# Kernel optimization log

Hardware: AMD Instinct MI355X
Metric: run time of the kernel (lower is better)

The kernel has to match this reference:

```python
import jax, jax.numpy as jnp
import numpy as np

B, N, C, H, W = 4, 5, 64, 96, 288
DOWNSAMPLE_RATE = 4
DISCRETE_RATIO = 0.4
DECAY_WEIGHTS = jax.nn.softmax(jnp.array([1.0, 0.5], dtype=jnp.float32))  # frame=1, decay=0.5


def _warp_one(img, theta):
    # img: (C,H,W), theta: (2,3). Matches F.affine_grid + F.grid_sample
    # (bilinear, zeros padding, align_corners=True).
    c, h, w = img.shape
    xs = jnp.linspace(-1.0, 1.0, w, dtype=img.dtype)
    ys = jnp.linspace(-1.0, 1.0, h, dtype=img.dtype)
    gy, gx = jnp.meshgrid(ys, xs, indexing='ij')
    base = jnp.stack([gx.ravel(), gy.ravel(), jnp.ones(h * w, img.dtype)], 0)  # (3, HW)
    g = theta @ base  # (2, HW) normalized coords
    px = (g[0] + 1.0) * 0.5 * (w - 1)
    py = (g[1] + 1.0) * 0.5 * (h - 1)
    x0 = jnp.floor(px); y0 = jnp.floor(py)
    wx = px - x0; wy = py - y0
    def tap(yy, xx):
        yi = jnp.clip(yy, 0, h - 1).astype(jnp.int32)
        xi = jnp.clip(xx, 0, w - 1).astype(jnp.int32)
        valid = ((yy >= 0) & (yy <= h - 1) & (xx >= 0) & (xx <= w - 1)).astype(img.dtype)
        return img[:, yi, xi] * valid  # (C, HW)
    out = (tap(y0, x0) * (1 - wx) * (1 - wy)
           + tap(y0, x0 + 1) * wx * (1 - wy)
           + tap(y0 + 1, x0) * (1 - wx) * wy
           + tap(y0 + 1, x0 + 1) * wx * wy)
    return out.reshape(c, h, w)


def _frame_score(hist, mlp_w, mlp_b):
    # hist: (B,N,C,H,W) -> per-pixel ego-vs-neighbor attention score (B,N,1,H,W).
    b, n, c, h, w = hist.shape
    node = hist.reshape(b, n, c, h * w).transpose(0, 3, 1, 2)  # (B, P, N, C)
    ego = node[:, :, 0]          # (B, P, C)
    neigh = node[:, :, 1:]       # (B, P, N-1, C)
    # Query rows are all the repeated ego vector -> one row suffices (identical math).
    s = jnp.einsum('bpc,bpkc->bpk', ego, neigh) / jnp.sqrt(jnp.asarray(c, hist.dtype))
    attn = jax.nn.softmax(s, axis=-1)
    ctx = jnp.einsum('bpk,bpkc->bpc', attn, neigh)
    sc = jax.nn.sigmoid(ctx @ mlp_w.T + mlp_b)                   # (B, P, 1)
    sc = jnp.broadcast_to(sc[:, :, None, :], (b, h * w, n - 1, 1))
    ego_sc = jnp.ones((b, h * w, 1, 1), hist.dtype)
    overall = jnp.concatenate([ego_sc, sc], axis=2)              # (B, P, N, 1)
    return overall.transpose(0, 2, 3, 1).reshape(b, n, 1, h, w)


def _forward(x0, x1, pairwise_t_matrix, mlp_w, mlp_b):
    x0g = x0.reshape(B, N, C, H, W)
    x1g = x1.reshape(B, N, C, H, W)

    # --- TemporalSampling: weighted per-frame scores, threshold, 3x3 max-pool ---
    conf = DECAY_WEIGHTS[0] * _frame_score(x0g, mlp_w, mlp_b) \
         + DECAY_WEIGHTS[1] * _frame_score(x1g, mlp_w, mlp_b)      # (B,N,1,H,W)
    mask = jnp.where(conf > 0.5, jnp.float32(1.0), jnp.float32(0.0))
    mask = jax.lax.reduce_window(mask, -jnp.inf, jax.lax.max,
                                 (1, 1, 1, 3, 3), (1, 1, 1, 1, 1), 'SAME')
    x = x0g * mask  # broadcast over C

    # --- normalize pairwise transform to 2x3 affine matrices ---
    t = pairwise_t_matrix[:, :, :, jnp.array([0, 1])][:, :, :, :, jnp.array([0, 1, 3])]  # (B,L,L,2,3)
    t = t.at[..., 0, 1].mul(H / W)
    t = t.at[..., 1, 0].mul(W / H)
    t = t.at[..., 0, 2].set(t[..., 0, 2] / (DOWNSAMPLE_RATE * DISCRETE_RATIO * W) * 2)
    t = t.at[..., 1, 2].set(t[..., 1, 2] / (DOWNSAMPLE_RATE * DISCRETE_RATIO * H) * 2)
    theta = t[:, 0]  # (B,N,2,3): warp each cav into ego frame

    # --- per-agent warp ---
    warped = jax.vmap(jax.vmap(_warp_one))(x, theta)  # (B,N,C,H,W)

    # --- AttenFusion: per-pixel NxN attention, keep ego row ---
    nf = warped.reshape(B, N, C, H * W).transpose(0, 3, 1, 2)  # (B, P, N, C)
    s = jnp.einsum('bpc,bpkc->bpk', nf[:, :, 0], nf) / jnp.sqrt(jnp.asarray(C, nf.dtype))
    attn = jax.nn.softmax(s, axis=-1)
    ctx = jnp.einsum('bpk,bpkc->bpc', attn, nf)                 # (B, P, C)
    x_fuse = ctx.transpose(0, 2, 1).reshape(B, C, H, W)
    return x_fuse


def setup_inputs() -> dict:
    key = jax.random.key(0)
    k0, k1, k2, k3 = jax.random.split(key, 4)
    x0 = jax.random.normal(k0, (B * N, C, H, W), dtype=jnp.float32)
    x1 = jax.random.normal(k1, (B * N, C, H, W), dtype=jnp.float32)
    eye = jnp.broadcast_to(jnp.eye(4, dtype=jnp.float32), (B, N, N, 4, 4))
    pairwise_t_matrix = eye + 0.01 * jax.random.normal(k2, (B, N, N, 4, 4), dtype=jnp.float32)
    mlp_w = 0.1 * jax.random.normal(k3, (1, C), dtype=jnp.float32)
    mlp_b = jnp.zeros((1,), dtype=jnp.float32)
    record_len = jnp.full((B,), N, dtype=jnp.int32)
    return {"x0": x0, "x1": x1, "pairwise_t_matrix": pairwise_t_matrix,
            "mlp_w": mlp_w, "mlp_b": mlp_b, "record_len": record_len}


def reference(x0, x1, pairwise_t_matrix, mlp_w, mlp_b, record_len):
    # record_len is uniform (=N) and only determines the static regrouping.
    return _forward(x0, x1, pairwise_t_matrix, mlp_w, mlp_b)
```

## Files before the change

kernel.cpp:

```cpp
#include <hip/hip_runtime.h>
#include <cmath>

#define BB 4
#define NN 5
#define CC 64
#define HH 96
#define WW 288
#define PP (HH*WW)
#define QP (PP/4)
#define BP (BB*PP)
#define BQ (BP/4)
#define TPITCH 65


static __device__ __forceinline__ float sigmoidf_(float x) {
    return 1.0f / (1.0f + expf(-x));
}
static __device__ __forceinline__ float4 f4zero() {
    return make_float4(0.f, 0.f, 0.f, 0.f);
}
static __device__ __forceinline__ void fma4s(float4& a, float s, const float4& v) {
    a.x += s * v.x; a.y += s * v.y; a.z += s * v.z; a.w += s * v.w;
}
static __device__ __forceinline__ void fma44(float4& a, const float4& s, const float4& v) {
    a.x += s.x * v.x; a.y += s.y * v.y; a.z += s.z * v.z; a.w += s.w * v.w;
}
static __device__ __forceinline__ float dot4(const float4& a, const float4& b) {
    return a.x*b.x + a.y*b.y + a.z*b.z + a.w*b.w;
}
static __device__ __forceinline__ float score4(const float* dd, const float* mm, float bias) {
    float s0 = dd[0]*0.125f, s1 = dd[1]*0.125f, s2 = dd[2]*0.125f, s3 = dd[3]*0.125f;
    float mx = fmaxf(fmaxf(s0, s1), fmaxf(s2, s3));
    float e0 = expf(s0-mx), e1 = expf(s1-mx), e2 = expf(s2-mx), e3 = expf(s3-mx);
    float inv = 1.0f / (e0+e1+e2+e3);
    float z = (e0*mm[0] + e1*mm[1] + e2*mm[2] + e3*mm[3]) * inv + bias;
    return sigmoidf_(z);
}

static __device__ __forceinline__ void theta_load(
    const float* __restrict__ pmat, int b, int n,
    float& t00, float& t01, float& t02, float& t10, float& t11, float& t12)
{
    const float* m = pmat + ((size_t)(b * NN + 0) * NN + n) * 16;
    t00 = m[0];
    t01 = m[1] * ((float)HH / (float)WW);
    t02 = m[3] * (float)(2.0 / (4.0 * 0.4 * (double)WW));
    t10 = m[4] * ((float)WW / (float)HH);
    t11 = m[5];
    t12 = m[7] * (float)(2.0 / (4.0 * 0.4 * (double)HH));
}

__global__ __launch_bounds__(256) void x1_part_kernel(
    const float4* __restrict__ x1, const float* __restrict__ mlp_w,
    float4* __restrict__ dpart1)
{
    int q   = blockIdx.x * 256 + threadIdx.x;
    int seg = blockIdx.y;
    int b  = q / QP;
    int qp = q - b * QP;
    const float4* base = x1 + (size_t)b * (NN*CC*QP) + qp;

    float4 d[4] = {f4zero(), f4zero(), f4zero(), f4zero()};
    float4 m[4] = {f4zero(), f4zero(), f4zero(), f4zero()};
    #pragma unroll 4
    for (int ci = 0; ci < 16; ci++) {
        int c = seg * 16 + ci;
        float4 e  = base[(size_t)c * QP];
        float  wc = mlp_w[c];
        #pragma unroll
        for (int k = 1; k < NN; k++) {
            float4 v = base[((size_t)k * CC + c) * QP];
            fma44(d[k-1], e, v);
            fma4s(m[k-1], wc, v);
        }
    }
    #pragma unroll
    for (int j = 0; j < 4; j++) {
        dpart1[((size_t)seg * 8 + j)     * BQ + q] = d[j];
        dpart1[((size_t)seg * 8 + 4 + j) * BQ + q] = m[j];
    }
}

__global__ __launch_bounds__(256) void transpose_mask_kernel(
    const float4* __restrict__ x0f4, const float* __restrict__ mlp_w,
    float4* __restrict__ x0t, float* __restrict__ dpx0)
{
    __shared__ float A[64 * TPITCH];
    __shared__ float Bsh[64 * TPITCH];
    __shared__ float redD[256];
    __shared__ float redM[256];
    __shared__ float wlds[64];

    int t   = threadIdx.x;
    int b   = blockIdx.y;
    int pt0 = blockIdx.x * 64;
    int c   = t >> 2, pq = t & 3;
    int pix = t >> 2, cg = t & 3;

    if (t < 64) wlds[t] = mlp_w[t];

    {
        const float4* src = x0f4 + ((size_t)(b*NN + 0) * CC + c) * QP
                                 + blockIdx.x * 16 + pq * 4;
        float4 r[4];
        #pragma unroll
        for (int j = 0; j < 4; j++) r[j] = src[j];
        #pragma unroll
        for (int j = 0; j < 4; j++) {
            int col = pq * 16 + j * 4;
            A[c*TPITCH + col+0] = r[j].x;
            A[c*TPITCH + col+1] = r[j].y;
            A[c*TPITCH + col+2] = r[j].z;
            A[c*TPITCH + col+3] = r[j].w;
        }
    }
    __syncthreads();
    float a[16];
    {
        #pragma unroll
        for (int j = 0; j < 16; j++) a[j] = A[(cg*16 + j)*TPITCH + pix];
        float4* dst = x0t + ((size_t)(b*NN + 0) * PP + pt0 + pix) * 16 + cg * 4;
        #pragma unroll
        for (int jj = 0; jj < 4; jj++)
            dst[jj] = make_float4(a[jj*4+0], a[jj*4+1], a[jj*4+2], a[jj*4+3]);
    }

    for (int k = 1; k < NN; k++) {
        const float4* src = x0f4 + ((size_t)(b*NN + k) * CC + c) * QP
                                 + blockIdx.x * 16 + pq * 4;
        float4 r[4];
        #pragma unroll
        for (int j = 0; j < 4; j++) r[j] = src[j];
        __syncthreads();
        #pragma unroll
        for (int j = 0; j < 4; j++) {
            int col = pq * 16 + j * 4;
            Bsh[c*TPITCH + col+0] = r[j].x;
            Bsh[c*TPITCH + col+1] = r[j].y;
            Bsh[c*TPITCH + col+2] = r[j].z;
            Bsh[c*TPITCH + col+3] = r[j].w;
        }
        __syncthreads();
        float bv[16];
        #pragma unroll
        for (int j = 0; j < 16; j++) bv[j] = Bsh[(cg*16 + j)*TPITCH + pix];
        float4* dst = x0t + ((size_t)(b*NN + k) * PP + pt0 + pix) * 16 + cg * 4;
        #pragma unroll
        for (int jj = 0; jj < 4; jj++)
            dst[jj] = make_float4(bv[jj*4+0], bv[jj*4+1], bv[jj*4+2], bv[jj*4+3]);

        float sd = 0.f, sm = 0.f;
        #pragma unroll
        for (int j = 0; j < 16; j++) {
            sd += a[j] * bv[j];
            sm += wlds[cg*16 + j] * bv[j];
        }
        redD[t] = sd;
        redM[t] = sm;
        __syncthreads();
        if (t < 64) {
            float dd = redD[t*4] + redD[t*4+1] + redD[t*4+2] + redD[t*4+3];
            float mm = redM[t*4] + redM[t*4+1] + redM[t*4+2] + redM[t*4+3];
            int gp = b * PP + pt0 + t;
            dpx0[(size_t)(k-1)   * BP + gp] = dd;
            dpx0[(size_t)(4+k-1) * BP + gp] = mm;
        }
    }
}

__global__ __launch_bounds__(256) void comb_kernel(
    const float4* __restrict__ dpart1, const float4* __restrict__ dpx0,
    const float* __restrict__ mlp_b, float4* __restrict__ premask)
{
    int q = blockIdx.x * 256 + threadIdx.x;
    float bias = mlp_b[0];

    float4 d1[8];
    #pragma unroll
    for (int j = 0; j < 8; j++) {
        float4 s = f4zero();
        #pragma unroll
        for (int seg = 0; seg < 4; seg++) {
            float4 v = dpart1[((size_t)seg * 8 + j) * BQ + q];
            s.x += v.x; s.y += v.y; s.z += v.z; s.w += v.w;
        }
        d1[j] = s;
    }
    float4 d0[8];
    #pragma unroll
    for (int j = 0; j < 8; j++) d0[j] = dpx0[(size_t)j * BQ + q];

    const float W0 = 0.6224593312018546f, W1 = 0.3775406687981454f;
    float4 res;
    #pragma unroll
    for (int kcomp = 0; kcomp < 4; kcomp++) {
        float dd0[4], mm0[4], dd1[4], mm1[4];
        #pragma unroll
        for (int j = 0; j < 4; j++) {
            dd0[j] = ((const float*)&d0[j])[kcomp];
            mm0[j] = ((const float*)&d0[4+j])[kcomp];
            dd1[j] = ((const float*)&d1[j])[kcomp];
            mm1[j] = ((const float*)&d1[4+j])[kcomp];
        }
        float sc0 = score4(dd0, mm0, bias);
        float sc1 = score4(dd1, mm1, bias);
        float conf = W0 * sc0 + W1 * sc1;
        ((float*)&res)[kcomp] = (conf > 0.5f) ? 1.f : 0.f;
    }
    premask[q] = res;
}

__global__ __launch_bounds__(256) void pool_kernel(
    const float* __restrict__ pre, float4* __restrict__ pooled)
{
    int q  = blockIdx.x * 256 + threadIdx.x;
    int b  = q / QP;
    int qp = q - b * QP;
    int p0 = qp * 4;
    int h  = p0 / WW;
    int w0 = p0 - h * WW;
    const float* pb = pre + (size_t)b * PP;
    float m[4] = {0.f, 0.f, 0.f, 0.f};
    #pragma unroll
    for (int dy = -1; dy <= 1; dy++) {
        int y = h + dy;
        if (y < 0 || y >= HH) continue;
        const float* row = pb + y * WW;
        float c_[6];
        float4 mid = *(const float4*)(row + w0);
        c_[0] = (w0 > 0) ? row[w0 - 1] : 0.f;
        c_[1] = mid.x; c_[2] = mid.y; c_[3] = mid.z; c_[4] = mid.w;
        c_[5] = (w0 + 4 < WW) ? row[w0 + 4] : 0.f;
        #pragma unroll
        for (int j = 0; j < 4; j++)
            m[j] = fmaxf(m[j], fmaxf(c_[j], fmaxf(c_[j+1], c_[j+2])));
    }
    pooled[q] = make_float4(m[0], m[1], m[2], m[3]);
}

__global__ __launch_bounds__(256) void fuse_kernel(
    const float4* __restrict__ x0t, const float* __restrict__ pmat,
    const float* __restrict__ pooled, float* __restrict__ out)
{
    int g   = blockIdx.x * 256 + threadIdx.x;
    int pix = g >> 4;
    int cq  = g & 15;
    int b = pix / PP;
    int p = pix - b * PP;
    int h = p / WW;
    int w = p - h * WW;

    float gx = -1.0f + 2.0f * (float)w / (float)(WW - 1);
    float gy = -1.0f + 2.0f * (float)h / (float)(HH - 1);
    const float* poolb = pooled + (size_t)b * PP;

    float4 wv[NN];
    #pragma unroll
    for (int n = 0; n < NN; n++) {
        float t00, t01, t02, t10, t11, t12;
        theta_load(pmat, b, n, t00, t01, t02, t10, t11, t12);
        float g0 = t00 * gx + t01 * gy + t02;
        float g1 = t10 * gx + t11 * gy + t12;
        float fx = (g0 + 1.0f) * 0.5f * (float)(WW - 1);
        float fy = (g1 + 1.0f) * 0.5f * (float)(HH - 1);
        float x0f = floorf(fx), y0f = floorf(fy);
        float wx = fx - x0f, wy = fy - y0f;
        float bw[4] = { (1.f - wx) * (1.f - wy), wx * (1.f - wy),
                        (1.f - wx) * wy,         wx * wy };
        const float4* fr = x0t + (size_t)(b * NN + n) * PP * 16;
        float4 acc = f4zero();
        #pragma unroll
        for (int t = 0; t < 4; t++) {
            float xx = (t & 1) ? (x0f + 1.0f) : x0f;
            float yy = (t >> 1) ? (y0f + 1.0f) : y0f;
            int xi = min(max((int)xx, 0), WW - 1);
            int yi = min(max((int)yy, 0), HH - 1);
            float valid = (yy >= 0.0f && yy <= (float)(HH - 1) &&
                           xx >= 0.0f && xx <= (float)(WW - 1)) ? 1.0f : 0.0f;
            int off = yi * WW + xi;
            float mk = (n == 0) ? 1.0f : poolb[off];
            float wgt = bw[t] * valid * mk;
            float4 v = fr[(size_t)off * 16 + cq];
            fma4s(acc, wgt, v);
        }
        wv[n] = acc;
    }

    float dt[NN];
    #pragma unroll
    for (int n = 0; n < NN; n++) dt[n] = dot4(wv[0], wv[n]);
    #pragma unroll
    for (int n = 0; n < NN; n++) {
        #pragma unroll
        for (int msk = 1; msk < 16; msk <<= 1)
            dt[n] += __shfl_xor(dt[n], msk, 16);
    }

    float s[NN], attn[NN];
    float mx = -INFINITY;
    #pragma unroll
    for (int n = 0; n < NN; n++) { s[n] = dt[n] * 0.125f; mx = fmaxf(mx, s[n]); }
    float sum = 0.f;
    #pragma unroll
    for (int n = 0; n < NN; n++) { attn[n] = expf(s[n] - mx); sum += attn[n]; }
    float inv = 1.0f / sum;

    float4 o = f4zero();
    #pragma unroll
    for (int n = 0; n < NN; n++) fma4s(o, attn[n] * inv, wv[n]);

    size_t ob = ((size_t)(b * CC + cq * 4)) * PP + p;
    out[ob]                = o.x;
    out[ob + (size_t)PP]   = o.y;
    out[ob + (size_t)2*PP] = o.z;
    out[ob + (size_t)3*PP] = o.w;
}

extern "C" void kernel_launch(void* const* d_in, const int* in_sizes, int n_in,
                              void* d_out, int out_size, void* d_ws, size_t ws_size,
                              hipStream_t stream) {
    float*       x0    = (float*)d_in[0];
    float*       x1    = (float*)d_in[1];
    const float* pmat  = (const float*)d_in[2];
    const float* mlp_w = (const float*)d_in[3];
    const float* mlp_b = (const float*)d_in[4];
    float* out = (float*)d_out;

    float4* x0f4    = (float4*)x0;
    float4* x1f4    = (float4*)x1;
    float4* out4    = (float4*)out;
    float4* dpart1  = out4;
    float*  dpx0_f  = out + (size_t)128 * BQ;
    float4* dpx0_4  = (float4*)dpx0_f;
    float4* x0t     = x1f4;
    float*  pre_f   = x0;
    float4* pre_4   = x0f4;
    float*  pool_f  = x0 + (size_t)BP;
    float4* pool_4  = (float4*)pool_f;

    dim3 blk(256);
    x1_part_kernel       <<<dim3(BQ/256, 4),  blk, 0, stream>>>(x1f4, mlp_w, dpart1);
    transpose_mask_kernel<<<dim3(PP/64, BB),  blk, 0, stream>>>(x0f4, mlp_w, x0t, dpx0_f);
    comb_kernel          <<<dim3(BQ/256),     blk, 0, stream>>>(dpart1, dpx0_4, mlp_b, pre_4);
    pool_kernel          <<<dim3(BQ/256),     blk, 0, stream>>>(pre_f, pool_4);
    fuse_kernel          <<<dim3(BP/16),      blk, 0, stream>>>(x0t, pmat, pool_f, out);
}
```

Baseline: 389.4 us.

## Fuse x1 reduction and x0 transpose into one launch, swizzle fuse blocks

```diff
diff --git a/kernel.cpp b/kernel.cpp
--- a/kernel.cpp
+++ b/kernel.cpp
@@ -50,12 +50,11 @@
     t12 = m[7] * (float)(2.0 / (4.0 * 0.4 * (double)HH));
 }
 
-__global__ __launch_bounds__(256) void x1_part_kernel(
+static __device__ __forceinline__ void x1_part_body(
+    int q, int seg,
     const float4* __restrict__ x1, const float* __restrict__ mlp_w,
     float4* __restrict__ dpart1)
 {
-    int q   = blockIdx.x * 256 + threadIdx.x;
-    int seg = blockIdx.y;
     int b  = q / QP;
     int qp = q - b * QP;
     const float4* base = x1 + (size_t)b * (NN*CC*QP) + qp;
@@ -81,19 +80,23 @@
     }
 }
 
-__global__ __launch_bounds__(256) void transpose_mask_kernel(
+__global__ __launch_bounds__(256) void x1_part_kernel(
+    const float4* __restrict__ x1, const float* __restrict__ mlp_w,
+    float4* __restrict__ dpart1)
+{
+    int q   = blockIdx.x * 256 + threadIdx.x;
+    int seg = blockIdx.y;
+    x1_part_body(q, seg, x1, mlp_w, dpart1);
+}
+
+static __device__ __forceinline__ void transpose_mask_body(
+    int tile, int b,
     const float4* __restrict__ x0f4, const float* __restrict__ mlp_w,
-    float4* __restrict__ x0t, float* __restrict__ dpx0)
-{
-    __shared__ float A[64 * TPITCH];
-    __shared__ float Bsh[64 * TPITCH];
-    __shared__ float redD[256];
-    __shared__ float redM[256];
-    __shared__ float wlds[64];
-
+    float4* __restrict__ x0t, float* __restrict__ dpx0,
+    float* A, float* Bsh, float* redD, float* redM, float* wlds)
+{
     int t   = threadIdx.x;
-    int b   = blockIdx.y;
-    int pt0 = blockIdx.x * 64;
+    int pt0 = tile * 64;
     int c   = t >> 2, pq = t & 3;
     int pix = t >> 2, cg = t & 3;
 
@@ -101,7 +104,7 @@
 
     {
         const float4* src = x0f4 + ((size_t)(b*NN + 0) * CC + c) * QP
-                                 + blockIdx.x * 16 + pq * 4;
+                                 + tile * 16 + pq * 4;
         float4 r[4];
         #pragma unroll
         for (int j = 0; j < 4; j++) r[j] = src[j];
@@ -127,7 +130,7 @@
 
     for (int k = 1; k < NN; k++) {
         const float4* src = x0f4 + ((size_t)(b*NN + k) * CC + c) * QP
-                                 + blockIdx.x * 16 + pq * 4;
+                                 + tile * 16 + pq * 4;
         float4 r[4];
         #pragma unroll
         for (int j = 0; j < 4; j++) r[j] = src[j];
@@ -168,6 +171,45 @@
     }
 }
 
+__global__ __launch_bounds__(256) void transpose_mask_kernel(
+    const float4* __restrict__ x0f4, const float* __restrict__ mlp_w,
+    float4* __restrict__ x0t, float* __restrict__ dpx0)
+{
+    __shared__ float A[64 * TPITCH];
+    __shared__ float Bsh[64 * TPITCH];
+    __shared__ float redD[256];
+    __shared__ float redM[256];
+    __shared__ float wlds[64];
+    transpose_mask_body(blockIdx.x, blockIdx.y, x0f4, mlp_w, x0t, dpx0,
+                        A, Bsh, redD, redM, wlds);
+}
+
+__global__ __launch_bounds__(256) void stage1_fused(
+    const float4* __restrict__ x0f4, const float4* __restrict__ x1f4,
+    const float* __restrict__ mlp_w, float4* __restrict__ x0t,
+    float* __restrict__ dpx0, float4* __restrict__ dpart1)
+{
+    __shared__ float A[64 * TPITCH];
+    __shared__ float Bsh[64 * TPITCH];
+    __shared__ float redD[256];
+    __shared__ float redM[256];
+    __shared__ float wlds[64];
+
+    int bid = blockIdx.x;
+    if (bid < 432) {
+        int seg = bid / 108;
+        int qb  = bid - seg * 108;
+        int q   = qb * 256 + threadIdx.x;
+        x1_part_body(q, seg, x1f4, mlp_w, dpart1);
+    } else {
+        int id   = bid - 432;
+        int b    = id / 432;
+        int tile = id - b * 432;
+        transpose_mask_body(tile, b, x0f4, mlp_w, x0t, dpx0,
+                            A, Bsh, redD, redM, wlds);
+    }
+}
+
 __global__ __launch_bounds__(256) void comb_kernel(
     const float4* __restrict__ dpart1, const float4* __restrict__ dpx0,
     const float* __restrict__ mlp_b, float4* __restrict__ premask)
@@ -242,11 +284,13 @@
     const float4* __restrict__ x0t, const float* __restrict__ pmat,
     const float* __restrict__ pooled, float* __restrict__ out)
 {
-    int g   = blockIdx.x * 256 + threadIdx.x;
-    int pix = g >> 4;
-    int cq  = g & 15;
-    int b = pix / PP;
-    int p = pix - b * PP;
+    int bid = blockIdx.x;
+    int swz = (bid & 7) * (BP/16/8) + (bid >> 3);
+    int pix0 = swz * 16;
+    int b  = pix0 / PP;
+    int p0 = pix0 - b * PP;
+    int cq = threadIdx.x & 15;
+    int p  = p0 + (threadIdx.x >> 4);
     int h = p / WW;
     int w = p - h * WW;
 
@@ -280,8 +324,10 @@
             int off = yi * WW + xi;
             float mk = (n == 0) ? 1.0f : poolb[off];
             float wgt = bw[t] * valid * mk;
-            float4 v = fr[(size_t)off * 16 + cq];
-            fma4s(acc, wgt, v);
+            if (wgt != 0.0f) {
+                float4 v = fr[(size_t)off * 16 + cq];
+                fma4s(acc, wgt, v);
+            }
         }
         wv[n] = acc;
     }
@@ -332,16 +378,28 @@
     float4* dpart1  = out4;
     float*  dpx0_f  = out + (size_t)128 * BQ;
     float4* dpx0_4  = (float4*)dpx0_f;
-    float4* x0t     = x1f4;
     float*  pre_f   = x0;
     float4* pre_4   = x0f4;
     float*  pool_f  = x0 + (size_t)BP;
     float4* pool_4  = (float4*)pool_f;
 
+    const size_t x0t_bytes = (size_t)BB * NN * PP * CC * sizeof(float);
+    bool use_ws = (d_ws != nullptr) && (ws_size >= x0t_bytes);
+
     dim3 blk(256);
-    x1_part_kernel       <<<dim3(BQ/256, 4),  blk, 0, stream>>>(x1f4, mlp_w, dpart1);
-    transpose_mask_kernel<<<dim3(PP/64, BB),  blk, 0, stream>>>(x0f4, mlp_w, x0t, dpx0_f);
-    comb_kernel          <<<dim3(BQ/256),     blk, 0, stream>>>(dpart1, dpx0_4, mlp_b, pre_4);
-    pool_kernel          <<<dim3(BQ/256),     blk, 0, stream>>>(pre_f, pool_4);
-    fuse_kernel          <<<dim3(BP/16),      blk, 0, stream>>>(x0t, pmat, pool_f, out);
-}
+    if (use_ws) {
+        float4* x0t = (float4*)d_ws;
+        stage1_fused <<<dim3(432 + 1728), blk, 0, stream>>>(
+            x0f4, x1f4, mlp_w, x0t, dpx0_f, dpart1);
+        comb_kernel  <<<dim3(BQ/256), blk, 0, stream>>>(dpart1, dpx0_4, mlp_b, pre_4);
+        pool_kernel  <<<dim3(BQ/256), blk, 0, stream>>>(pre_f, pool_4);
+        fuse_kernel  <<<dim3(BP/16),  blk, 0, stream>>>(x0t, pmat, pool_f, out);
+    } else {
+        float4* x0t = x1f4;
+        x1_part_kernel       <<<dim3(BQ/256, 4),  blk, 0, stream>>>(x1f4, mlp_w, dpart1);
+        transpose_mask_kernel<<<dim3(PP/64, BB),  blk, 0, stream>>>(x0f4, mlp_w, x0t, dpx0_f);
+        comb_kernel          <<<dim3(BQ/256),     blk, 0, stream>>>(dpart1, dpx0_4, mlp_b, pre_4);
+        pool_kernel          <<<dim3(BQ/256),     blk, 0, stream>>>(pre_f, pool_4);
+        fuse_kernel          <<<dim3(BP/16),      blk, 0, stream>>>(x0t, pmat, pool_f, out);
+    }
+}
```

Result: slower. 412.3 us (+5.9%).

## Drop x0 transpose; gather directly from channel-major x0 in fuse kernel

Applied to the files above, without the earlier changes.

```diff
diff --git a/kernel.cpp b/kernel.cpp
--- a/kernel.cpp
+++ b/kernel.cpp
@@ -10,7 +10,6 @@
 #define QP (PP/4)
 #define BP (BB*PP)
 #define BQ (BP/4)
-#define TPITCH 65
 
 
 static __device__ __forceinline__ float sigmoidf_(float x) {
@@ -24,9 +23,6 @@
 }
 static __device__ __forceinline__ void fma44(float4& a, const float4& s, const float4& v) {
     a.x += s.x * v.x; a.y += s.y * v.y; a.z += s.z * v.z; a.w += s.w * v.w;
-}
-static __device__ __forceinline__ float dot4(const float4& a, const float4& b) {
-    return a.x*b.x + a.y*b.y + a.z*b.z + a.w*b.w;
 }
 static __device__ __forceinline__ float score4(const float* dd, const float* mm, float bias) {
     float s0 = dd[0]*0.125f, s1 = dd[1]*0.125f, s2 = dd[2]*0.125f, s3 = dd[3]*0.125f;
@@ -50,15 +46,14 @@
     t12 = m[7] * (float)(2.0 / (4.0 * 0.4 * (double)HH));
 }
 
-__global__ __launch_bounds__(256) void x1_part_kernel(
-    const float4* __restrict__ x1, const float* __restrict__ mlp_w,
-    float4* __restrict__ dpart1)
-{
-    int q   = blockIdx.x * 256 + threadIdx.x;
-    int seg = blockIdx.y;
+static __device__ __forceinline__ void part_body(
+    int q, int seg,
+    const float4* __restrict__ src, const float* __restrict__ mlp_w,
+    float4* __restrict__ dst)
+{
     int b  = q / QP;
     int qp = q - b * QP;
-    const float4* base = x1 + (size_t)b * (NN*CC*QP) + qp;
+    const float4* base = src + (size_t)b * (NN*CC*QP) + qp;
 
     float4 d[4] = {f4zero(), f4zero(), f4zero(), f4zero()};
     float4 m[4] = {f4zero(), f4zero(), f4zero(), f4zero()};
@@ -76,119 +71,43 @@
     }
     #pragma unroll
     for (int j = 0; j < 4; j++) {
-        dpart1[((size_t)seg * 8 + j)     * BQ + q] = d[j];
-        dpart1[((size_t)seg * 8 + 4 + j) * BQ + q] = m[j];
-    }
-}
-
-__global__ __launch_bounds__(256) void transpose_mask_kernel(
-    const float4* __restrict__ x0f4, const float* __restrict__ mlp_w,
-    float4* __restrict__ x0t, float* __restrict__ dpx0)
-{
-    __shared__ float A[64 * TPITCH];
-    __shared__ float Bsh[64 * TPITCH];
-    __shared__ float redD[256];
-    __shared__ float redM[256];
-    __shared__ float wlds[64];
-
-    int t   = threadIdx.x;
-    int b   = blockIdx.y;
-    int pt0 = blockIdx.x * 64;
-    int c   = t >> 2, pq = t & 3;
-    int pix = t >> 2, cg = t & 3;
-
-    if (t < 64) wlds[t] = mlp_w[t];
-
-    {
-        const float4* src = x0f4 + ((size_t)(b*NN + 0) * CC + c) * QP
-                                 + blockIdx.x * 16 + pq * 4;
-        float4 r[4];
-        #pragma unroll
-        for (int j = 0; j < 4; j++) r[j] = src[j];
-        #pragma unroll
-        for (int j = 0; j < 4; j++) {
-            int col = pq * 16 + j * 4;
-            A[c*TPITCH + col+0] = r[j].x;
-            A[c*TPITCH + col+1] = r[j].y;
-            A[c*TPITCH + col+2] = r[j].z;
-            A[c*TPITCH + col+3] = r[j].w;
-        }
-    }
-    __syncthreads();
-    float a[16];
-    {
-        #pragma unroll
-        for (int j = 0; j < 16; j++) a[j] = A[(cg*16 + j)*TPITCH + pix];
-        float4* dst = x0t + ((size_t)(b*NN + 0) * PP + pt0 + pix) * 16 + cg * 4;
-        #pragma unroll
-        for (int jj = 0; jj < 4; jj++)
-            dst[jj] = make_float4(a[jj*4+0], a[jj*4+1], a[jj*4+2], a[jj*4+3]);
-    }
-
-    for (int k = 1; k < NN; k++) {
-        const float4* src = x0f4 + ((size_t)(b*NN + k) * CC + c) * QP
-                                 + blockIdx.x * 16 + pq * 4;
-        float4 r[4];
-        #pragma unroll
-        for (int j = 0; j < 4; j++) r[j] = src[j];
-        __syncthreads();
-        #pragma unroll
-        for (int j = 0; j < 4; j++) {
-            int col = pq * 16 + j * 4;
-            Bsh[c*TPITCH + col+0] = r[j].x;
-            Bsh[c*TPITCH + col+1] = r[j].y;
-            Bsh[c*TPITCH + col+2] = r[j].z;
-            Bsh[c*TPITCH + col+3] = r[j].w;
-        }
-        __syncthreads();
-        float bv[16];
-        #pragma unroll
-        for (int j = 0; j < 16; j++) bv[j] = Bsh[(cg*16 + j)*TPITCH + pix];
-        float4* dst = x0t + ((size_t)(b*NN + k) * PP + pt0 + pix) * 16 + cg * 4;
-        #pragma unroll
-        for (int jj = 0; jj < 4; jj++)
-            dst[jj] = make_float4(bv[jj*4+0], bv[jj*4+1], bv[jj*4+2], bv[jj*4+3]);
-
-        float sd = 0.f, sm = 0.f;
-        #pragma unroll
-        for (int j = 0; j < 16; j++) {
-            sd += a[j] * bv[j];
-            sm += wlds[cg*16 + j] * bv[j];
-        }
-        redD[t] = sd;
-        redM[t] = sm;
-        __syncthreads();
-        if (t < 64) {
-            float dd = redD[t*4] + redD[t*4+1] + redD[t*4+2] + redD[t*4+3];
-            float mm = redM[t*4] + redM[t*4+1] + redM[t*4+2] + redM[t*4+3];
-            int gp = b * PP + pt0 + t;
-            dpx0[(size_t)(k-1)   * BP + gp] = dd;
-            dpx0[(size_t)(4+k-1) * BP + gp] = mm;
-        }
-    }
+        dst[((size_t)seg * 8 + j)     * BQ + q] = d[j];
+        dst[((size_t)seg * 8 + 4 + j) * BQ + q] = m[j];
+    }
+}
+
+__global__ __launch_bounds__(256) void part_kernel(
+    const float4* __restrict__ x0, const float4* __restrict__ x1,
+    const float* __restrict__ mlp_w,
+    float4* __restrict__ dpart0, float4* __restrict__ dpart1)
+{
+    int q    = blockIdx.x * 256 + threadIdx.x;
+    int seg8 = blockIdx.y;
+    if (seg8 < 4) part_body(q, seg8,     x1, mlp_w, dpart1);
+    else          part_body(q, seg8 - 4, x0, mlp_w, dpart0);
 }
 
 __global__ __launch_bounds__(256) void comb_kernel(
-    const float4* __restrict__ dpart1, const float4* __restrict__ dpx0,
+    const float4* __restrict__ dpart0, const float4* __restrict__ dpart1,
     const float* __restrict__ mlp_b, float4* __restrict__ premask)
 {
     int q = blockIdx.x * 256 + threadIdx.x;
     float bias = mlp_b[0];
 
-    float4 d1[8];
+    float4 d0[8], d1[8];
     #pragma unroll
     for (int j = 0; j < 8; j++) {
-        float4 s = f4zero();
+        float4 s0 = f4zero(), s1 = f4zero();
         #pragma unroll
         for (int seg = 0; seg < 4; seg++) {
-            float4 v = dpart1[((size_t)seg * 8 + j) * BQ + q];
-            s.x += v.x; s.y += v.y; s.z += v.z; s.w += v.w;
-        }
-        d1[j] = s;
-    }
-    float4 d0[8];
-    #pragma unroll
-    for (int j = 0; j < 8; j++) d0[j] = dpx0[(size_t)j * BQ + q];
+            float4 v0 = dpart0[((size_t)seg * 8 + j) * BQ + q];
+            float4 v1 = dpart1[((size_t)seg * 8 + j) * BQ + q];
+            s0.x += v0.x; s0.y += v0.y; s0.z += v0.z; s0.w += v0.w;
+            s1.x += v1.x; s1.y += v1.y; s1.z += v1.z; s1.w += v1.w;
+        }
+        d0[j] = s0;
+        d1[j] = s1;
+    }
 
     const float W0 = 0.6224593312018546f, W1 = 0.3775406687981454f;
     float4 res;
@@ -238,15 +157,18 @@
     pooled[q] = make_float4(m[0], m[1], m[2], m[3]);
 }
 
-__global__ __launch_bounds__(256) void fuse_kernel(
-    const float4* __restrict__ x0t, const float* __restrict__ pmat,
+__global__ __launch_bounds__(256) void fuse_gather_kernel(
+    const float* __restrict__ x0, const float* __restrict__ pmat,
     const float* __restrict__ pooled, float* __restrict__ out)
 {
-    int g   = blockIdx.x * 256 + threadIdx.x;
-    int pix = g >> 4;
-    int cq  = g & 15;
-    int b = pix / PP;
-    int p = pix - b * PP;
+    int bid = blockIdx.x;
+    int swz = (bid & 7) * (BP/64/8) + (bid >> 3);
+    int pix0 = swz * 64;
+    int b  = pix0 / PP;
+    int p0 = pix0 - b * PP;
+    int lane4 = threadIdx.x & 3;
+    int pi    = threadIdx.x >> 2;
+    int p = p0 + pi;
     int h = p / WW;
     int w = p - h * WW;
 
@@ -254,7 +176,8 @@
     float gy = -1.0f + 2.0f * (float)h / (float)(HH - 1);
     const float* poolb = pooled + (size_t)b * PP;
 
-    float4 wv[NN];
+    int   off[NN][4];
+    float wgt[NN][4];
     #pragma unroll
     for (int n = 0; n < NN; n++) {
         float t00, t01, t02, t10, t11, t12;
@@ -267,8 +190,6 @@
         float wx = fx - x0f, wy = fy - y0f;
         float bw[4] = { (1.f - wx) * (1.f - wy), wx * (1.f - wy),
                         (1.f - wx) * wy,         wx * wy };
-        const float4* fr = x0t + (size_t)(b * NN + n) * PP * 16;
-        float4 acc = f4zero();
         #pragma unroll
         for (int t = 0; t < 4; t++) {
             float xx = (t & 1) ? (x0f + 1.0f) : x0f;
@@ -277,23 +198,37 @@
             int yi = min(max((int)yy, 0), HH - 1);
             float valid = (yy >= 0.0f && yy <= (float)(HH - 1) &&
                            xx >= 0.0f && xx <= (float)(WW - 1)) ? 1.0f : 0.0f;
-            int off = yi * WW + xi;
-            float mk = (n == 0) ? 1.0f : poolb[off];
-            float wgt = bw[t] * valid * mk;
-            float4 v = fr[(size_t)off * 16 + cq];
-            fma4s(acc, wgt, v);
-        }
-        wv[n] = acc;
-    }
-
-    float dt[NN];
-    #pragma unroll
-    for (int n = 0; n < NN; n++) dt[n] = dot4(wv[0], wv[n]);
+            off[n][t] = yi * WW + xi;
+            float mk = (n == 0) ? 1.0f : poolb[off[n][t]];
+            wgt[n][t] = bw[t] * valid * mk;
+        }
+    }
+
+    const float* base = x0 + ((size_t)b * NN * CC + (size_t)lane4 * 16) * PP;
+
+    float dt[NN] = {0.f, 0.f, 0.f, 0.f, 0.f};
+    #pragma unroll 2
+    for (int ci = 0; ci < 16; ci++) {
+        const float* cb = base + (size_t)ci * PP;
+        float v0 = 0.f;
+        #pragma unroll
+        for (int t = 0; t < 4; t++)
+            if (wgt[0][t] != 0.f) v0 += wgt[0][t] * cb[off[0][t]];
+        dt[0] += v0 * v0;
+        #pragma unroll
+        for (int n = 1; n < NN; n++) {
+            const float* fb = cb + (size_t)n * CC * PP;
+            float v = 0.f;
+            #pragma unroll
+            for (int t = 0; t < 4; t++)
+                if (wgt[n][t] != 0.f) v += wgt[n][t] * fb[off[n][t]];
+            dt[n] += v0 * v;
+        }
+    }
     #pragma unroll
     for (int n = 0; n < NN; n++) {
-        #pragma unroll
-        for (int msk = 1; msk < 16; msk <<= 1)
-            dt[n] += __shfl_xor(dt[n], msk, 16);
+        dt[n] += __shfl_xor(dt[n], 1, 64);
+        dt[n] += __shfl_xor(dt[n], 2, 64);
     }
 
     float s[NN], attn[NN];
@@ -304,16 +239,25 @@
     #pragma unroll
     for (int n = 0; n < NN; n++) { attn[n] = expf(s[n] - mx); sum += attn[n]; }
     float inv = 1.0f / sum;
-
-    float4 o = f4zero();
-    #pragma unroll
-    for (int n = 0; n < NN; n++) fma4s(o, attn[n] * inv, wv[n]);
-
-    size_t ob = ((size_t)(b * CC + cq * 4)) * PP + p;
-    out[ob]                = o.x;
-    out[ob + (size_t)PP]   = o.y;
-    out[ob + (size_t)2*PP] = o.z;
-    out[ob + (size_t)3*PP] = o.w;
+    #pragma unroll
+    for (int n = 0; n < NN; n++) attn[n] *= inv;
+
+    #pragma unroll 2
+    for (int ci = 0; ci < 16; ci++) {
+        const float* cb = base + (size_t)ci * PP;
+        float o = 0.f;
+        #pragma unroll
+        for (int n = 0; n < NN; n++) {
+            const float* fb = cb + (size_t)n * CC * PP;
+            float v = 0.f;
+            #pragma unroll
+            for (int t = 0; t < 4; t++)
+                if (wgt[n][t] != 0.f) v += wgt[n][t] * fb[off[n][t]];
+            o += attn[n] * v;
+        }
+        int c = lane4 * 16 + ci;
+        out[((size_t)(b * CC + c)) * PP + p] = o;
+    }
 }
 
 extern "C" void kernel_launch(void* const* d_in, const int* in_sizes, int n_in,
@@ -326,22 +270,33 @@
     const float* mlp_b = (const float*)d_in[4];
     float* out = (float*)d_out;
 
-    float4* x0f4    = (float4*)x0;
-    float4* x1f4    = (float4*)x1;
-    float4* out4    = (float4*)out;
-    float4* dpart1  = out4;
-    float*  dpx0_f  = out + (size_t)128 * BQ;
-    float4* dpx0_4  = (float4*)dpx0_f;
-    float4* x0t     = x1f4;
-    float*  pre_f   = x0;
-    float4* pre_4   = x0f4;
-    float*  pool_f  = x0 + (size_t)BP;
-    float4* pool_4  = (float4*)pool_f;
+    float4* x0f4 = (float4*)x0;
+    float4* x1f4 = (float4*)x1;
+
+    const size_t need_ws = (size_t)66 * BP * sizeof(float);
+    bool use_ws = (d_ws != nullptr) && (ws_size >= need_ws);
+
+    float *dpart1_f, *dpart0_f, *pre_f, *pool_f;
+    if (use_ws) {
+        float* ws = (float*)d_ws;
+        dpart1_f = ws;
+        dpart0_f = ws + (size_t)32 * BP;
+        pre_f    = ws + (size_t)64 * BP;
+        pool_f   = ws + (size_t)65 * BP;
+    } else {
+        dpart1_f = out;
+        dpart0_f = out + (size_t)32 * BP;
+        pre_f    = x1;
+        pool_f   = x1 + (size_t)BP;
+    }
+    float4* dpart1 = (float4*)dpart1_f;
+    float4* dpart0 = (float4*)dpart0_f;
+    float4* pre_4  = (float4*)pre_f;
+    float4* pool_4 = (float4*)pool_f;
 
     dim3 blk(256);
-    x1_part_kernel       <<<dim3(BQ/256, 4),  blk, 0, stream>>>(x1f4, mlp_w, dpart1);
-    transpose_mask_kernel<<<dim3(PP/64, BB),  blk, 0, stream>>>(x0f4, mlp_w, x0t, dpx0_f);
-    comb_kernel          <<<dim3(BQ/256),     blk, 0, stream>>>(dpart1, dpx0_4, mlp_b, pre_4);
-    pool_kernel          <<<dim3(BQ/256),     blk, 0, stream>>>(pre_f, pool_4);
-    fuse_kernel          <<<dim3(BP/16),      blk, 0, stream>>>(x0t, pmat, pool_f, out);
-}
+    part_kernel      <<<dim3(BQ/256, 8), blk, 0, stream>>>(x0f4, x1f4, mlp_w, dpart0, dpart1);
+    comb_kernel      <<<dim3(BQ/256),    blk, 0, stream>>>(dpart0, dpart1, mlp_b, pre_4);
+    pool_kernel      <<<dim3(BQ/256),    blk, 0, stream>>>(pre_f, pool_4);
+    fuse_gather_kernel<<<dim3(BP/64),    blk, 0, stream>>>(x0, pmat, pool_f, out);
+}
```

Result: slower. 641.4 us (+64.7%).
